# Kernel tuning notes

Hardware: AMD Instinct MI355X
Metric: run time of the kernel (lower is better)

Reference implementation:

```python
import jax, jax.numpy as jnp
import numpy as np

ALPHA = 0.5      # GCN2Conv alpha
THETA = 1.0      # GCN2Conv theta (beta_l = log(theta/l + 1))
EPS = 1e-5       # pyg LayerNorm eps
N_LAYERS = 8
N, E, DIN, DHID, DOUT = 50000, 800000, 128, 256, 128


def setup_inputs() -> dict:
    key = jax.random.key(0)
    ks = jax.random.split(key, 10)
    x = jax.random.normal(ks[0], (N, DIN), jnp.float32)
    edge_index = jax.random.randint(ks[1], (2, E), 0, N, dtype=jnp.int32)
    lin1_w = jax.random.normal(ks[2], (DIN, DHID), jnp.float32) / np.sqrt(DIN)
    lin1_b = jnp.zeros((DHID,), jnp.float32)
    conv_w1 = jax.random.normal(ks[3], (N_LAYERS, DHID, DHID), jnp.float32) / np.sqrt(DHID)
    conv_w2 = jax.random.normal(ks[4], (N_LAYERS, DHID, DHID), jnp.float32) / np.sqrt(DHID)
    norm_gamma = jnp.ones((N_LAYERS, DHID), jnp.float32)
    norm_beta = jnp.zeros((N_LAYERS, DHID), jnp.float32)
    lin2_w = jax.random.normal(ks[5], (DHID, DOUT), jnp.float32) / np.sqrt(DHID)
    lin2_b = jnp.zeros((DOUT,), jnp.float32)
    return {"x": x, "edge_index": edge_index, "lin1_w": lin1_w, "lin1_b": lin1_b,
            "conv_w1": conv_w1, "conv_w2": conv_w2, "norm_gamma": norm_gamma,
            "norm_beta": norm_beta, "lin2_w": lin2_w, "lin2_b": lin2_b}


def _gcn_norm(edge_index, n_nodes, dtype):
    # add self loops, then symmetric deg^{-1/2} A_hat deg^{-1/2} normalization
    loop = jnp.arange(n_nodes, dtype=edge_index.dtype)
    row = jnp.concatenate([edge_index[0], loop])
    col = jnp.concatenate([edge_index[1], loop])
    deg = jax.ops.segment_sum(jnp.ones_like(row, dtype=dtype), col, num_segments=n_nodes)
    dis = jnp.where(deg > 0, jax.lax.rsqrt(jnp.maximum(deg, 1e-12)), 0.0)
    return row, col, dis[row] * dis[col]


def _graph_layernorm(h, gamma, beta):
    # pyg LayerNorm mode='graph', batch=None: normalize over all nodes+features
    z = h - jnp.mean(h)
    z = z / (jnp.sqrt(jnp.mean(z * z)) + EPS)
    return gamma * z + beta


def reference(x, edge_index, lin1_w, lin1_b, conv_w1, conv_w2, norm_gamma, norm_beta, lin2_w, lin2_b):
    n_nodes = x.shape[0]
    row, col, enorm = _gcn_norm(edge_index, n_nodes, x.dtype)
    # lin1 + relu (dropout p=0 -> identity); residual=None -> zeros
    x0 = jax.nn.relu(x @ lin1_w + lin1_b)
    h = x0
    for i in range(conv_w1.shape[0]):
        beta_l = float(np.log(THETA / (i + 1) + 1.0))
        # sparse neighborhood aggregation: out[c] += norm * h[r]
        agg = jax.ops.segment_sum(h[row] * enorm[:, None], col, num_segments=n_nodes)
        t = (1.0 - ALPHA) * agg          # propagated part
        r = ALPHA * x0                   # initial-residual part (res = x0 + zeros)
        # shared_weights=False: separate weights for propagated and residual parts
        h = (1.0 - beta_l) * (t + r) + beta_l * (t @ conv_w1[i] + r @ conv_w2[i])
        h = jax.nn.relu(_graph_layernorm(h, norm_gamma[i], norm_beta[i]))
    return jax.nn.relu(h @ lin2_w + lin2_b)
```

## Files before the change

kernel.cpp:

```cpp
#include <hip/hip_runtime.h>
#include <hip/hip_bf16.h>
#include <math.h>

#define DIN 128
#define DH 256
#define DOUT 128
#define NLAYERS 8
#define EPSLN 1e-5f

typedef __hip_bfloat16 bf16;
typedef __attribute__((ext_vector_type(8))) short short8;
typedef __attribute__((ext_vector_type(4))) short short4v;
typedef __attribute__((ext_vector_type(4))) float f32x4;

__device__ __forceinline__ float ldf(const void* p, size_t idx, int isbf) {
    if (isbf) return __bfloat162float(((const bf16*)p)[idx]);
    return ((const float*)p)[idx];
}
__device__ __forceinline__ short f2s(float v) {
    bf16 b = __float2bfloat16(v);
    return *reinterpret_cast<short*>(&b);
}
__device__ __forceinline__ float s2f(short s) {
    unsigned int u = ((unsigned int)(unsigned short)s) << 16;
    float f;
    __builtin_memcpy(&f, &u, 4);
    return f;
}
__device__ __forceinline__ void gl_lds16(const void* g, void* l) {
    __builtin_amdgcn_global_load_lds(
        (const __attribute__((address_space(1))) unsigned int*)g,
        (__attribute__((address_space(3))) unsigned int*)l,
        16, 0, 0);
}

__global__ void k_detect(const unsigned int* __restrict__ xw, int* __restrict__ flag) {
    __shared__ int cnt;
    if (threadIdx.x == 0) cnt = 0;
    __syncthreads();
    unsigned int w = xw[threadIdx.x];
    int e = (w >> 7) & 0xFF;
    if (e >= 112 && e <= 140) atomicAdd(&cnt, 1);
    __syncthreads();
    if (threadIdx.x == 0) *flag = (cnt >= 128) ? 1 : 0;
}

__global__ void k_init_cnt(int* __restrict__ cnt, float* __restrict__ stats, int N) {
    int i = blockIdx.x * blockDim.x + threadIdx.x;
    if (i < N) cnt[i] = 0;
    if (blockIdx.x == 0 && threadIdx.x < 16) stats[threadIdx.x] = 0.0f;
}
__global__ void k_count(const int* __restrict__ cols, int* __restrict__ cnt, int E) {
    int e = blockIdx.x * blockDim.x + threadIdx.x;
    if (e < E) atomicAdd(&cnt[cols[e]], 1);
}
__global__ void k_dis(const int* __restrict__ cnt, float* __restrict__ dis, int N) {
    int i = blockIdx.x * blockDim.x + threadIdx.x;
    if (i < N) dis[i] = rsqrtf(1.0f + (float)cnt[i]);
}
__global__ void k_scan1(const int* __restrict__ cnt, int* __restrict__ rowptr,
                        int* __restrict__ bsum, int N) {
    __shared__ int s[256];
    int t = threadIdx.x;
    int i = blockIdx.x * 256 + t;
    s[t] = (i < N) ? cnt[i] : 0;
    __syncthreads();
    for (int off = 1; off < 256; off <<= 1) {
        int x = (t >= off) ? s[t - off] : 0;
        __syncthreads();
        s[t] += x;
        __syncthreads();
    }
    if (i < N) rowptr[i + 1] = s[t];
    if (t == 255) bsum[blockIdx.x] = s[255];
}
__global__ void k_scan2(int* __restrict__ bsum, int nb) {
    __shared__ int s[256];
    int t = threadIdx.x;
    s[t] = (t < nb) ? bsum[t] : 0;
    __syncthreads();
    for (int off = 1; off < 256; off <<= 1) {
        int x = (t >= off) ? s[t - off] : 0;
        __syncthreads();
        s[t] += x;
        __syncthreads();
    }
    if (t < nb) bsum[t] = s[t];
}
__global__ void k_scan3(int* __restrict__ rowptr, const int* __restrict__ bsum,
                        int* __restrict__ cursor, int N) {
    int i = blockIdx.x * 256 + threadIdx.x;
    if (i == 0) { rowptr[0] = 0; cursor[0] = 0; }
    if (i < N) {
        int v = rowptr[i + 1] + ((blockIdx.x > 0) ? bsum[blockIdx.x - 1] : 0);
        rowptr[i + 1] = v;
        cursor[i + 1] = v;
    }
}
__global__ void k_fill(const int* __restrict__ rows, const int* __restrict__ cols,
                       int* __restrict__ cursor, int* __restrict__ csr, int E) {
    int e = blockIdx.x * blockDim.x + threadIdx.x;
    if (e < E) {
        int c = cols[e], r = rows[e];
        int pos = atomicAdd(&cursor[c], 1);
        csr[pos] = r;
    }
}

__global__ void k_transw2(const void* __restrict__ w1, const void* __restrict__ w2,
                          const int* __restrict__ flag, short* __restrict__ wt) {
    __shared__ float tile[32][33];
    int z = blockIdx.z;
    int lay = z >> 1, m = z & 1;
    const void* src = m ? w2 : w1;
    size_t sbase = (size_t)lay * 65536;
    short* dst = wt + (size_t)lay * 131072 + (size_t)m * 256;
    float bl = logf(1.0f / (float)(lay + 1) + 1.0f);
    float c0 = 0.5f * (1.0f - bl);
    float c1 = 0.5f * bl;
    int isbf = *flag;
    int tx = threadIdx.x, ty = threadIdx.y;
    int n0 = blockIdx.x * 32, k0 = blockIdx.y * 32;
    #pragma unroll
    for (int i = 0; i < 4; i++) {
        int k = k0 + ty + i * 8;
        tile[ty + i * 8][tx] = ldf(src, sbase + (size_t)k * 256 + n0 + tx, isbf);
    }
    __syncthreads();
    #pragma unroll
    for (int i = 0; i < 4; i++) {
        int n = n0 + ty + i * 8;
        int k = k0 + tx;
        float v = c1 * tile[tx][ty + i * 8];
        if (k == n) v += c0;
        dst[(size_t)n * 512 + k] = f2s(v);
    }
}

__global__ void k_transw_lin(const void* __restrict__ src, const int* __restrict__ flag,
                             short* __restrict__ dst, int K, int Nc) {
    __shared__ float tile[32][33];
    int isbf = *flag;
    int tx = threadIdx.x, ty = threadIdx.y;
    int n0 = blockIdx.x * 32, k0 = blockIdx.y * 32;
    #pragma unroll
    for (int i = 0; i < 4; i++) {
        int k = k0 + ty + i * 8;
        tile[ty + i * 8][tx] = ldf(src, (size_t)k * Nc + n0 + tx, isbf);
    }
    __syncthreads();
    #pragma unroll
    for (int i = 0; i < 4; i++) {
        int n = n0 + ty + i * 8;
        dst[(size_t)n * K + k0 + tx] = f2s(tile[tx][ty + i * 8]);
    }
}

__global__ void k_convx(const void* __restrict__ x, const int* __restrict__ flag,
                        short* __restrict__ xb, int total) {
    int i = blockIdx.x * 256 + threadIdx.x;
    if (i < total) xb[i] = f2s(ldf(x, i, *flag));
}

template<int KK, int FINAL, int TRANSA>
__global__ __launch_bounds__(256) void gemm_mfma(
    const short* __restrict__ A, const short* __restrict__ wt,
    const void* __restrict__ bias, const int* __restrict__ flag,
    const void* __restrict__ g, const void* __restrict__ b, size_t loff,
    const float* __restrict__ stats2, float invTotal,
    void* __restrict__ outp, int Nn)
{
    __shared__ __align__(16) short Atile[128 * 32];
    __shared__ __align__(16) short Btile[128 * 32];
    int t = threadIdx.x;
    int w = t >> 6, lane = t & 63;
    int lr = lane & 15, quad = lane >> 4;
    int row0 = blockIdx.x * 128;
    int col0 = blockIdx.y * 128;
    int ncols = gridDim.y * 128;
    int sub = t & 3;
    int srow = t >> 2;
    const int isbf = *flag;
    float mu = 0.f, inv = 0.f;
    if (TRANSA) {
        mu = stats2[0] * invTotal;
        float var = stats2[1] * invTotal - mu * mu;
        var = var > 0.f ? var : 0.f;
        inv = 1.0f / (sqrtf(var) + EPSLN);
    }
    f32x4 acc[2][8];
    #pragma unroll
    for (int m = 0; m < 2; m++)
        #pragma unroll
        for (int nt = 0; nt < 8; nt++)
            #pragma unroll
            for (int j = 0; j < 4; j++) acc[m][nt][j] = 0.f;

    for (int kb = 0; kb < KK; kb += 32) {
        #pragma unroll
        for (int r = 0; r < 2; r++) {
            int gr = row0 + srow + r * 64;
            if (gr >= Nn) gr = Nn - 1;
            if (TRANSA) {
                short8 av = *(const short8*)(A + (size_t)gr * KK + kb + sub * 8);
                short8 tv;
                #pragma unroll
                for (int j = 0; j < 8; j++) {
                    int kc = kb + sub * 8 + j;
                    float gg = ldf(g, loff + kc, isbf);
                    float bb = ldf(b, loff + kc, isbf);
                    float v = fmaf(gg * inv, s2f(av[j]), fmaf(-gg * inv, mu, bb));
                    v = v > 0.f ? v : 0.f;
                    tv[j] = f2s(v);
                }
                *(short8*)(Atile + (size_t)(t + r * 256) * 8) = tv;
            } else {
                gl_lds16(A + (size_t)gr * KK + kb + sub * 8,
                         Atile + (size_t)(t + r * 256) * 8);
            }
        }
        #pragma unroll
        for (int r = 0; r < 2; r++) {
            int n = col0 + srow + r * 64;
            gl_lds16(wt + (size_t)n * KK + kb + sub * 8,
                     Btile + (size_t)(t + r * 256) * 8);
        }
        __syncthreads();
        short8 a0 = *(const short8*)(Atile + (w * 32 + lr) * 32 + quad * 8);
        short8 a1 = *(const short8*)(Atile + (w * 32 + 16 + lr) * 32 + quad * 8);
        #pragma unroll
        for (int nt = 0; nt < 8; nt++) {
            short8 bv = *(const short8*)(Btile + (nt * 16 + lr) * 32 + quad * 8);
            acc[0][nt] = __builtin_amdgcn_mfma_f32_16x16x32_bf16(a0, bv, acc[0][nt], 0, 0, 0);
            acc[1][nt] = __builtin_amdgcn_mfma_f32_16x16x32_bf16(a1, bv, acc[1][nt], 0, 0, 0);
        }
        __syncthreads();
    }
    #pragma unroll
    for (int m = 0; m < 2; m++) {
        #pragma unroll
        for (int nt = 0; nt < 8; nt++) {
            int gc = col0 + nt * 16 + lr;
            float bb = ldf(bias, gc, isbf);
            #pragma unroll
            for (int i = 0; i < 4; i++) {
                int gr = row0 + w * 32 + m * 16 + quad * 4 + i;
                if (gr < Nn) {
                    float v = acc[m][nt][i] + bb;
                    v = v > 0.f ? v : 0.f;
                    size_t off = (size_t)gr * ncols + gc;
                    if (FINAL) {
                        if (isbf) ((bf16*)outp)[off] = __float2bfloat16(v);
                        else      ((float*)outp)[off] = v;
                    } else {
                        ((bf16*)outp)[off] = __float2bfloat16(v);
                    }
                }
            }
        }
    }
}

__global__ __launch_bounds__(256) void k_gather5(
    const int* __restrict__ rowptr, const int* __restrict__ csr,
    const float* __restrict__ dis, const bf16* __restrict__ hsrc,
    bf16* __restrict__ agg,
    const void* __restrict__ g, const void* __restrict__ b, size_t loff,
    const float* __restrict__ stats2, float invTotal, int useLN,
    const int* __restrict__ flag, int N)
{
    int gid = blockIdx.x * 256 + threadIdx.x;
    int node = gid >> 6;
    if (node >= N) return;
    int col = (gid & 63) * 4;
    float cA[4], cB[4];
    if (useLN) {
        int isbf = *flag;
        float mu = stats2[0] * invTotal;
        float var = stats2[1] * invTotal - mu * mu;
        var = var > 0.f ? var : 0.f;
        float inv = 1.0f / (sqrtf(var) + EPSLN);
        #pragma unroll
        for (int j = 0; j < 4; j++) {
            float gg = ldf(g, loff + col + j, isbf);
            float bb = ldf(b, loff + col + j, isbf);
            cA[j] = gg * inv;
            cB[j] = fmaf(-gg * inv, mu, bb);
        }
    } else {
        #pragma unroll
        for (int j = 0; j < 4; j++) { cA[j] = 1.0f; cB[j] = 0.0f; }
    }
    const short* hs = (const short*)hsrc;
    float dc = dis[node];
    float a0[4], a1[4], a2[4], a3[4];
    {
        short4v hv = *(const short4v*)(hs + (size_t)node * DH + col);
        #pragma unroll
        for (int j = 0; j < 4; j++) {
            float v = fmaf(cA[j], s2f(hv[j]), cB[j]);
            v = v > 0.f ? v : 0.f;
            a0[j] = dc * v;
            a1[j] = 0.f; a2[j] = 0.f; a3[j] = 0.f;
        }
    }
    int i = rowptr[node], e1 = rowptr[node + 1];
    for (; i + 8 <= e1; i += 8) {
        int r0 = csr[i],     r1 = csr[i + 1], r2 = csr[i + 2], r3 = csr[i + 3];
        int r4 = csr[i + 4], r5 = csr[i + 5], r6 = csr[i + 6], r7 = csr[i + 7];
        float w0 = dis[r0], w1 = dis[r1], w2 = dis[r2], w3 = dis[r3];
        float w4 = dis[r4], w5 = dis[r5], w6 = dis[r6], w7 = dis[r7];
        short4v v0 = *(const short4v*)(hs + (size_t)r0 * DH + col);
        short4v v1 = *(const short4v*)(hs + (size_t)r1 * DH + col);
        short4v v2 = *(const short4v*)(hs + (size_t)r2 * DH + col);
        short4v v3 = *(const short4v*)(hs + (size_t)r3 * DH + col);
        short4v v4 = *(const short4v*)(hs + (size_t)r4 * DH + col);
        short4v v5 = *(const short4v*)(hs + (size_t)r5 * DH + col);
        short4v v6 = *(const short4v*)(hs + (size_t)r6 * DH + col);
        short4v v7 = *(const short4v*)(hs + (size_t)r7 * DH + col);
        #pragma unroll
        for (int j = 0; j < 4; j++) {
            float t0 = fmaf(cA[j], s2f(v0[j]), cB[j]); t0 = t0 > 0.f ? t0 : 0.f;
            float t1 = fmaf(cA[j], s2f(v1[j]), cB[j]); t1 = t1 > 0.f ? t1 : 0.f;
            float t2 = fmaf(cA[j], s2f(v2[j]), cB[j]); t2 = t2 > 0.f ? t2 : 0.f;
            float t3 = fmaf(cA[j], s2f(v3[j]), cB[j]); t3 = t3 > 0.f ? t3 : 0.f;
            float t4 = fmaf(cA[j], s2f(v4[j]), cB[j]); t4 = t4 > 0.f ? t4 : 0.f;
            float t5 = fmaf(cA[j], s2f(v5[j]), cB[j]); t5 = t5 > 0.f ? t5 : 0.f;
            float t6 = fmaf(cA[j], s2f(v6[j]), cB[j]); t6 = t6 > 0.f ? t6 : 0.f;
            float t7 = fmaf(cA[j], s2f(v7[j]), cB[j]); t7 = t7 > 0.f ? t7 : 0.f;
            a0[j] = fmaf(w0, t0, a0[j]);
            a1[j] = fmaf(w1, t1, a1[j]);
            a2[j] = fmaf(w2, t2, a2[j]);
            a3[j] = fmaf(w3, t3, a3[j]);
            a0[j] = fmaf(w4, t4, a0[j]);
            a1[j] = fmaf(w5, t5, a1[j]);
            a2[j] = fmaf(w6, t6, a2[j]);
            a3[j] = fmaf(w7, t7, a3[j]);
        }
    }
    for (; i + 2 <= e1; i += 2) {
        int r0 = csr[i], r1 = csr[i + 1];
        float w0 = dis[r0], w1 = dis[r1];
        short4v v0 = *(const short4v*)(hs + (size_t)r0 * DH + col);
        short4v v1 = *(const short4v*)(hs + (size_t)r1 * DH + col);
        #pragma unroll
        for (int j = 0; j < 4; j++) {
            float t0 = fmaf(cA[j], s2f(v0[j]), cB[j]); t0 = t0 > 0.f ? t0 : 0.f;
            float t1 = fmaf(cA[j], s2f(v1[j]), cB[j]); t1 = t1 > 0.f ? t1 : 0.f;
            a0[j] = fmaf(w0, t0, a0[j]);
            a1[j] = fmaf(w1, t1, a1[j]);
        }
    }
    for (; i < e1; i++) {
        int r = csr[i];
        float wr = dis[r];
        short4v v0 = *(const short4v*)(hs + (size_t)r * DH + col);
        #pragma unroll
        for (int j = 0; j < 4; j++) {
            float t0 = fmaf(cA[j], s2f(v0[j]), cB[j]); t0 = t0 > 0.f ? t0 : 0.f;
            a0[j] = fmaf(wr, t0, a0[j]);
        }
    }
    short4v o;
    #pragma unroll
    for (int j = 0; j < 4; j++) o[j] = f2s(dc * ((a0[j] + a1[j]) + (a2[j] + a3[j])));
    *(short4v*)((short*)agg + (size_t)node * DH + col) = o;
}

__global__ __launch_bounds__(256) void gemm_layer4(
    const bf16* __restrict__ agg, const bf16* __restrict__ x0,
    const short* __restrict__ wt, bf16* __restrict__ h,
    float* __restrict__ stats2, int Nn)
{
    __shared__ __align__(16) short Atile[128 * 32];
    __shared__ __align__(16) short Btile[128 * 32];
    __shared__ float red[512];
    int t = threadIdx.x;
    int w = t >> 6, lane = t & 63;
    int lr = lane & 15, quad = lane >> 4;
    int row0 = blockIdx.x * 128;
    int col0 = blockIdx.y * 128;
    int sub = t & 3;
    int srow = t >> 2;
    f32x4 acc[2][8];
    #pragma unroll
    for (int m = 0; m < 2; m++)
        #pragma unroll
        for (int nt = 0; nt < 8; nt++)
            #pragma unroll
            for (int j = 0; j < 4; j++) acc[m][nt][j] = 0.f;

    for (int kb = 0; kb < 512; kb += 32) {
        const short* Asrc = (const short*)((kb < DH) ? agg : x0);
        int ka = kb & (DH - 1);
        #pragma unroll
        for (int r = 0; r < 2; r++) {
            int gr = row0 + srow + r * 64;
            if (gr >= Nn) gr = Nn - 1;
            gl_lds16(Asrc + (size_t)gr * DH + ka + sub * 8,
                     Atile + (size_t)(t + r * 256) * 8);
        }
        #pragma unroll
        for (int r = 0; r < 2; r++) {
            int n = col0 + srow + r * 64;
            gl_lds16(wt + (size_t)n * 512 + kb + sub * 8,
                     Btile + (size_t)(t + r * 256) * 8);
        }
        __syncthreads();
        short8 a0 = *(const short8*)(Atile + (w * 32 + lr) * 32 + quad * 8);
        short8 a1 = *(const short8*)(Atile + (w * 32 + 16 + lr) * 32 + quad * 8);
        #pragma unroll
        for (int nt = 0; nt < 8; nt++) {
            short8 bv = *(const short8*)(Btile + (nt * 16 + lr) * 32 + quad * 8);
            acc[0][nt] = __builtin_amdgcn_mfma_f32_16x16x32_bf16(a0, bv, acc[0][nt], 0, 0, 0);
            acc[1][nt] = __builtin_amdgcn_mfma_f32_16x16x32_bf16(a1, bv, acc[1][nt], 0, 0, 0);
        }
        __syncthreads();
    }
    float lsum = 0.f, lsq = 0.f;
    #pragma unroll
    for (int m = 0; m < 2; m++) {
        #pragma unroll
        for (int nt = 0; nt < 8; nt++) {
            int gc = col0 + nt * 16 + lr;
            #pragma unroll
            for (int i = 0; i < 4; i++) {
                int gr = row0 + w * 32 + m * 16 + quad * 4 + i;
                if (gr < Nn) {
                    float v = acc[m][nt][i];
                    h[(size_t)gr * DH + gc] = __float2bfloat16(v);
                    lsum += v;
                    lsq += v * v;
                }
            }
        }
    }
    red[t] = lsum;
    red[256 + t] = lsq;
    __syncthreads();
    for (int s = 128; s > 0; s >>= 1) {
        if (t < s) { red[t] += red[t + s]; red[256 + t] += red[256 + t + s]; }
        __syncthreads();
    }
    if (t == 0) {
        atomicAdd(&stats2[0], red[0]);
        atomicAdd(&stats2[1], red[256]);
    }
}

extern "C" void kernel_launch(void* const* d_in, const int* in_sizes, int n_in,
                              void* d_out, int out_size, void* d_ws, size_t ws_size,
                              hipStream_t stream) {
    const void* x      = d_in[0];
    const int*  ei     = (const int*)d_in[1];
    const void* lin1_w = d_in[2];
    const void* lin1_b = d_in[3];
    const void* conv_w1= d_in[4];
    const void* conv_w2= d_in[5];
    const void* gam    = d_in[6];
    const void* bet    = d_in[7];
    const void* lin2_w = d_in[8];
    const void* lin2_b = d_in[9];

    const int N = in_sizes[0] / DIN;
    const int E = in_sizes[1] / 2;
    const int* rows = ei;
    const int* cols = ei + E;
    const size_t NDH = (size_t)N * DH;
    const size_t Nr = ((size_t)N + 255) / 256 * 256;

    char* p = (char*)d_ws;
    auto alloc = [&](size_t bytes) { char* q = p; p += (bytes + 255) & ~(size_t)255; return q; };
    float* dis    = (float*)alloc(Nr * 4);
    float* stats  = (float*)alloc(1024);
    int*   flag   = (int*)(stats + 16);
    int*   cnt    = (int*)alloc(Nr * 4);
    int*   rowptr = (int*)alloc((Nr + 256) * 4);
    int*   cursor = (int*)alloc((Nr + 256) * 4);
    int*   bsum   = (int*)alloc(1024);
    int*   csr    = (int*)alloc((size_t)E * 4);
    short* wt     = (short*)alloc((size_t)NLAYERS * 131072 * 2);
    short* w1t    = (short*)alloc((size_t)DH * DIN * 2);
    short* w2t    = (short*)alloc((size_t)DOUT * DH * 2);
    short* xb     = (short*)alloc((size_t)N * DIN * 2);
    bf16*  agg    = (bf16*)alloc(NDH * 2);
    bf16*  x0     = (bf16*)alloc(NDH * 2);
    bf16*  h      = (bf16*)alloc(NDH * 2);

    dim3 blk(256);
    int nbN = (N + 255) / 256;
    dim3 gN(nbN);
    dim3 gE((E + 255) / 256);
    dim3 gB128_2((N + 127) / 128, 2);
    dim3 gB128_1((N + 127) / 128, 1);
    dim3 gG((N + 3) / 4);
    dim3 gTW(8, 8, 16);
    dim3 bTW(32, 8);

    k_detect<<<1, 256, 0, stream>>>((const unsigned int*)x, flag);
    k_init_cnt<<<gN, blk, 0, stream>>>(cnt, stats, N);
    k_count<<<gE, blk, 0, stream>>>(cols, cnt, E);
    k_dis<<<gN, blk, 0, stream>>>(cnt, dis, N);
    k_scan1<<<gN, blk, 0, stream>>>(cnt, rowptr, bsum, N);
    k_scan2<<<1, 256, 0, stream>>>(bsum, nbN);
    k_scan3<<<gN, blk, 0, stream>>>(rowptr, bsum, cursor, N);
    k_fill<<<gE, blk, 0, stream>>>(rows, cols, cursor, csr, E);
    k_transw2<<<gTW, bTW, 0, stream>>>(conv_w1, conv_w2, flag, wt);
    k_transw_lin<<<dim3(DH / 32, DIN / 32), bTW, 0, stream>>>(lin1_w, flag, w1t, DIN, DH);
    k_transw_lin<<<dim3(DOUT / 32, DH / 32), bTW, 0, stream>>>(lin2_w, flag, w2t, DH, DOUT);
    k_convx<<<dim3((unsigned)(((size_t)N * DIN + 255) / 256)), blk, 0, stream>>>(x, flag, xb, N * DIN);

    gemm_mfma<DIN, 0, 0><<<gB128_2, blk, 0, stream>>>(xb, w1t, lin1_b, flag,
                                                      nullptr, nullptr, 0, stats, 0.f,
                                                      x0, N);

    const float invTotal = 1.0f / ((float)N * (float)DH);
    for (int l = 0; l < NLAYERS; l++) {
        const bf16* hsrc = (l == 0) ? x0 : h;
        size_t loff = (l == 0) ? 0 : (size_t)(l - 1) * DH;
        const float* st = (l == 0) ? stats : stats + 2 * (l - 1);
        k_gather5<<<gG, blk, 0, stream>>>(rowptr, csr, dis, hsrc, agg,
                                          gam, bet, loff, st, invTotal,
                                          l > 0 ? 1 : 0, flag, N);
        gemm_layer4<<<gB128_2, blk, 0, stream>>>(agg, x0, wt + (size_t)l * 131072,
                                                 h, stats + 2 * l, N);
    }
    gemm_mfma<DH, 1, 1><<<gB128_1, blk, 0, stream>>>((const short*)h, w2t, lin2_b, flag,
                                                     gam, bet, (size_t)(NLAYERS - 1) * DH,
                                                     stats + 2 * (NLAYERS - 1), invTotal,
                                                     d_out, N);
}
```

Measured before the change: 1.280 ms.

## Fuse all GCN2 layers into one persistent cooperative kernel with grid syncs

Replaces the per-layer gather and GEMM launches with a single cooperative persistent kernel. Each layer runs an in-place layernorm+ReLU pass over h, a wave-per-node gather, and a 64-row-tile MFMA GEMM, separated by grid-wide syncs. The goal is to remove the 16 kernel launches and their tail effects, but it adds an extra full read/write pass for normalisation and three grid barriers per layer. The smaller GEMM tile and a grid capped at 768 blocks may lower per-tile efficiency, and the fallback gather loses its 8-way unroll.

```diff
diff --git a/kernel.cpp b/kernel.cpp
--- a/kernel.cpp
+++ b/kernel.cpp
@@ -1,6 +1,9 @@
 #include <hip/hip_runtime.h>
+#include <hip/hip_cooperative_groups.h>
 #include <hip/hip_bf16.h>
 #include <math.h>
+
+namespace cg = cooperative_groups;
 
 #define DIN 128
 #define DH 256
@@ -293,7 +296,7 @@
     }
     const short* hs = (const short*)hsrc;
     float dc = dis[node];
-    float a0[4], a1[4], a2[4], a3[4];
+    float a0[4], a1[4];
     {
         short4v hv = *(const short4v*)(hs + (size_t)node * DH + col);
         #pragma unroll
@@ -301,43 +304,10 @@
             float v = fmaf(cA[j], s2f(hv[j]), cB[j]);
             v = v > 0.f ? v : 0.f;
             a0[j] = dc * v;
-            a1[j] = 0.f; a2[j] = 0.f; a3[j] = 0.f;
+            a1[j] = 0.f;
         }
     }
     int i = rowptr[node], e1 = rowptr[node + 1];
-    for (; i + 8 <= e1; i += 8) {
-        int r0 = csr[i],     r1 = csr[i + 1], r2 = csr[i + 2], r3 = csr[i + 3];
-        int r4 = csr[i + 4], r5 = csr[i + 5], r6 = csr[i + 6], r7 = csr[i + 7];
-        float w0 = dis[r0], w1 = dis[r1], w2 = dis[r2], w3 = dis[r3];
-        float w4 = dis[r4], w5 = dis[r5], w6 = dis[r6], w7 = dis[r7];
-        short4v v0 = *(const short4v*)(hs + (size_t)r0 * DH + col);
-        short4v v1 = *(const short4v*)(hs + (size_t)r1 * DH + col);
-        short4v v2 = *(const short4v*)(hs + (size_t)r2 * DH + col);
-        short4v v3 = *(const short4v*)(hs + (size_t)r3 * DH + col);
-        short4v v4 = *(const short4v*)(hs + (size_t)r4 * DH + col);
-        short4v v5 = *(const short4v*)(hs + (size_t)r5 * DH + col);
-        short4v v6 = *(const short4v*)(hs + (size_t)r6 * DH + col);
-        short4v v7 = *(const short4v*)(hs + (size_t)r7 * DH + col);
-        #pragma unroll
-        for (int j = 0; j < 4; j++) {
-            float t0 = fmaf(cA[j], s2f(v0[j]), cB[j]); t0 = t0 > 0.f ? t0 : 0.f;
-            float t1 = fmaf(cA[j], s2f(v1[j]), cB[j]); t1 = t1 > 0.f ? t1 : 0.f;
-            float t2 = fmaf(cA[j], s2f(v2[j]), cB[j]); t2 = t2 > 0.f ? t2 : 0.f;
-            float t3 = fmaf(cA[j], s2f(v3[j]), cB[j]); t3 = t3 > 0.f ? t3 : 0.f;
-            float t4 = fmaf(cA[j], s2f(v4[j]), cB[j]); t4 = t4 > 0.f ? t4 : 0.f;
-            float t5 = fmaf(cA[j], s2f(v5[j]), cB[j]); t5 = t5 > 0.f ? t5 : 0.f;
-            float t6 = fmaf(cA[j], s2f(v6[j]), cB[j]); t6 = t6 > 0.f ? t6 : 0.f;
-            float t7 = fmaf(cA[j], s2f(v7[j]), cB[j]); t7 = t7 > 0.f ? t7 : 0.f;
-            a0[j] = fmaf(w0, t0, a0[j]);
-            a1[j] = fmaf(w1, t1, a1[j]);
-            a2[j] = fmaf(w2, t2, a2[j]);
-            a3[j] = fmaf(w3, t3, a3[j]);
-            a0[j] = fmaf(w4, t4, a0[j]);
-            a1[j] = fmaf(w5, t5, a1[j]);
-            a2[j] = fmaf(w6, t6, a2[j]);
-            a3[j] = fmaf(w7, t7, a3[j]);
-        }
-    }
     for (; i + 2 <= e1; i += 2) {
         int r0 = csr[i], r1 = csr[i + 1];
         float w0 = dis[r0], w1 = dis[r1];
@@ -363,7 +333,7 @@
     }
     short4v o;
     #pragma unroll
-    for (int j = 0; j < 4; j++) o[j] = f2s(dc * ((a0[j] + a1[j]) + (a2[j] + a3[j])));
+    for (int j = 0; j < 4; j++) o[j] = f2s(dc * (a0[j] + a1[j]));
     *(short4v*)((short*)agg + (size_t)node * DH + col) = o;
 }
 
@@ -448,6 +418,186 @@
     }
 }
 
+__global__ __launch_bounds__(256, 2) void k_layers(
+    const int* __restrict__ rowptr, const int* __restrict__ csr,
+    const float* __restrict__ dis, const short* __restrict__ x0s,
+    short* __restrict__ hs, short* __restrict__ aggs,
+    const short* __restrict__ wt,
+    const void* __restrict__ gam, const void* __restrict__ bet,
+    float* __restrict__ stats, const int* __restrict__ flag,
+    float invTotal, int N)
+{
+    cg::grid_group grid = cg::this_grid();
+    __shared__ __align__(16) short Atile[64 * 32];
+    __shared__ __align__(16) short Btile[128 * 32];
+    __shared__ float red[512];
+    const int t = threadIdx.x;
+    const int w = t >> 6, lane = t & 63;
+    const int lr = lane & 15, quad = lane >> 4;
+    const int isbf = *flag;
+    const int nthreads = gridDim.x * 256;
+    const int gtid = blockIdx.x * 256 + t;
+    const int nwaves = gridDim.x * 4;
+    const int waveId = blockIdx.x * 4 + w;
+    const int srow = t >> 2, sub = t & 3;
+    const size_t NDH8 = (size_t)N * 32;
+    const int ntiles = ((N + 63) >> 6) * 2;
+
+    for (int l = 0; l < NLAYERS; ++l) {
+        if (l > 0) {
+            const float* st = stats + 2 * (l - 1);
+            size_t loff = (size_t)(l - 1) * DH;
+            float mu = st[0] * invTotal;
+            float var = st[1] * invTotal - mu * mu;
+            var = var > 0.f ? var : 0.f;
+            float inv = 1.0f / (sqrtf(var) + EPSLN);
+            for (size_t c = (size_t)gtid; c < NDH8; c += nthreads) {
+                int colb = (int)((c & 31) * 8);
+                short8 v = *(short8*)(hs + c * 8);
+                short8 o;
+                #pragma unroll
+                for (int j = 0; j < 8; j++) {
+                    float gg = ldf(gam, loff + colb + j, isbf);
+                    float bb = ldf(bet, loff + colb + j, isbf);
+                    float xv = fmaf(gg * inv, s2f(v[j]), fmaf(-gg * inv, mu, bb));
+                    xv = xv > 0.f ? xv : 0.f;
+                    o[j] = f2s(xv);
+                }
+                *(short8*)(hs + c * 8) = o;
+            }
+            __threadfence();
+            grid.sync();
+        }
+        {
+            const short* src = (l == 0) ? x0s : hs;
+            int col = lane * 4;
+            for (int node = waveId; node < N; node += nwaves) {
+                float dc = dis[node];
+                float a0[4], a1[4], a2[4], a3[4];
+                short4v hv = *(const short4v*)(src + (size_t)node * DH + col);
+                #pragma unroll
+                for (int j = 0; j < 4; j++) {
+                    a0[j] = dc * s2f(hv[j]);
+                    a1[j] = 0.f; a2[j] = 0.f; a3[j] = 0.f;
+                }
+                int i = rowptr[node], e1 = rowptr[node + 1];
+                for (; i + 8 <= e1; i += 8) {
+                    int r0 = csr[i],     r1 = csr[i + 1], r2 = csr[i + 2], r3 = csr[i + 3];
+                    int r4 = csr[i + 4], r5 = csr[i + 5], r6 = csr[i + 6], r7 = csr[i + 7];
+                    float w0 = dis[r0], w1 = dis[r1], w2 = dis[r2], w3 = dis[r3];
+                    float w4 = dis[r4], w5 = dis[r5], w6 = dis[r6], w7 = dis[r7];
+                    short4v v0 = *(const short4v*)(src + (size_t)r0 * DH + col);
+                    short4v v1 = *(const short4v*)(src + (size_t)r1 * DH + col);
+                    short4v v2 = *(const short4v*)(src + (size_t)r2 * DH + col);
+                    short4v v3 = *(const short4v*)(src + (size_t)r3 * DH + col);
+                    short4v v4 = *(const short4v*)(src + (size_t)r4 * DH + col);
+                    short4v v5 = *(const short4v*)(src + (size_t)r5 * DH + col);
+                    short4v v6 = *(const short4v*)(src + (size_t)r6 * DH + col);
+                    short4v v7 = *(const short4v*)(src + (size_t)r7 * DH + col);
+                    #pragma unroll
+                    for (int j = 0; j < 4; j++) {
+                        a0[j] = fmaf(w0, s2f(v0[j]), a0[j]);
+                        a1[j] = fmaf(w1, s2f(v1[j]), a1[j]);
+                        a2[j] = fmaf(w2, s2f(v2[j]), a2[j]);
+                        a3[j] = fmaf(w3, s2f(v3[j]), a3[j]);
+                        a0[j] = fmaf(w4, s2f(v4[j]), a0[j]);
+                        a1[j] = fmaf(w5, s2f(v5[j]), a1[j]);
+                        a2[j] = fmaf(w6, s2f(v6[j]), a2[j]);
+                        a3[j] = fmaf(w7, s2f(v7[j]), a3[j]);
+                    }
+                }
+                for (; i + 2 <= e1; i += 2) {
+                    int r0 = csr[i], r1 = csr[i + 1];
+                    float w0 = dis[r0], w1 = dis[r1];
+                    short4v v0 = *(const short4v*)(src + (size_t)r0 * DH + col);
+                    short4v v1 = *(const short4v*)(src + (size_t)r1 * DH + col);
+                    #pragma unroll
+                    for (int j = 0; j < 4; j++) {
+                        a0[j] = fmaf(w0, s2f(v0[j]), a0[j]);
+                        a1[j] = fmaf(w1, s2f(v1[j]), a1[j]);
+                    }
+                }
+                for (; i < e1; i++) {
+                    int r = csr[i];
+                    float wr = dis[r];
+                    short4v v0 = *(const short4v*)(src + (size_t)r * DH + col);
+                    #pragma unroll
+                    for (int j = 0; j < 4; j++) a0[j] = fmaf(wr, s2f(v0[j]), a0[j]);
+                }
+                short4v o;
+                #pragma unroll
+                for (int j = 0; j < 4; j++)
+                    o[j] = f2s(dc * ((a0[j] + a1[j]) + (a2[j] + a3[j])));
+                *(short4v*)(aggs + (size_t)node * DH + col) = o;
+            }
+        }
+        __threadfence();
+        grid.sync();
+        {
+            const short* wl = wt + (size_t)l * 131072;
+            float lsum = 0.f, lsq = 0.f;
+            for (int tile = blockIdx.x; tile < ntiles; tile += gridDim.x) {
+                int row0 = (tile >> 1) * 64;
+                int col0 = (tile & 1) * 128;
+                f32x4 acc[8];
+                #pragma unroll
+                for (int nt = 0; nt < 8; nt++)
+                    #pragma unroll
+                    for (int j = 0; j < 4; j++) acc[nt][j] = 0.f;
+                for (int kb = 0; kb < 512; kb += 32) {
+                    const short* Asrc = (kb < DH) ? aggs : x0s;
+                    int ka = kb & (DH - 1);
+                    int gr = row0 + srow;
+                    if (gr >= N) gr = N - 1;
+                    gl_lds16(Asrc + (size_t)gr * DH + ka + sub * 8,
+                             Atile + (size_t)t * 8);
+                    #pragma unroll
+                    for (int r = 0; r < 2; r++) {
+                        int n = col0 + srow + r * 64;
+                        gl_lds16(wl + (size_t)n * 512 + kb + sub * 8,
+                                 Btile + (size_t)(t + r * 256) * 8);
+                    }
+                    __syncthreads();
+                    short8 a0 = *(const short8*)(Atile + (w * 16 + lr) * 32 + quad * 8);
+                    #pragma unroll
+                    for (int nt = 0; nt < 8; nt++) {
+                        short8 bv = *(const short8*)(Btile + (nt * 16 + lr) * 32 + quad * 8);
+                        acc[nt] = __builtin_amdgcn_mfma_f32_16x16x32_bf16(a0, bv, acc[nt], 0, 0, 0);
+                    }
+                    __syncthreads();
+                }
+                #pragma unroll
+                for (int nt = 0; nt < 8; nt++) {
+                    int gc = col0 + nt * 16 + lr;
+                    #pragma unroll
+                    for (int i = 0; i < 4; i++) {
+                        int gr = row0 + w * 16 + quad * 4 + i;
+                        if (gr < N) {
+                            float v = acc[nt][i];
+                            hs[(size_t)gr * DH + gc] = f2s(v);
+                            lsum += v;
+                            lsq += v * v;
+                        }
+                    }
+                }
+            }
+            red[t] = lsum;
+            red[256 + t] = lsq;
+            __syncthreads();
+            for (int s = 128; s > 0; s >>= 1) {
+                if (t < s) { red[t] += red[t + s]; red[256 + t] += red[256 + t + s]; }
+                __syncthreads();
+            }
+            if (t == 0) {
+                atomicAdd(&stats[2 * l], red[0]);
+                atomicAdd(&stats[2 * l + 1], red[256]);
+            }
+        }
+        __threadfence();
+        grid.sync();
+    }
+}
+
 extern "C" void kernel_launch(void* const* d_in, const int* in_sizes, int n_in,
                               void* d_out, int out_size, void* d_ws, size_t ws_size,
                               hipStream_t stream) {
@@ -483,9 +633,9 @@
     short* w1t    = (short*)alloc((size_t)DH * DIN * 2);
     short* w2t    = (short*)alloc((size_t)DOUT * DH * 2);
     short* xb     = (short*)alloc((size_t)N * DIN * 2);
-    bf16*  agg    = (bf16*)alloc(NDH * 2);
-    bf16*  x0     = (bf16*)alloc(NDH * 2);
-    bf16*  h      = (bf16*)alloc(NDH * 2);
+    short* aggs   = (short*)alloc(NDH * 2);
+    short* x0s    = (short*)alloc(NDH * 2);
+    short* hs     = (short*)alloc(NDH * 2);
 
     dim3 blk(256);
     int nbN = (N + 255) / 256;
@@ -512,20 +662,52 @@
 
     gemm_mfma<DIN, 0, 0><<<gB128_2, blk, 0, stream>>>(xb, w1t, lin1_b, flag,
                                                       nullptr, nullptr, 0, stats, 0.f,
-                                                      x0, N);
-
-    const float invTotal = 1.0f / ((float)N * (float)DH);
-    for (int l = 0; l < NLAYERS; l++) {
-        const bf16* hsrc = (l == 0) ? x0 : h;
-        size_t loff = (l == 0) ? 0 : (size_t)(l - 1) * DH;
-        const float* st = (l == 0) ? stats : stats + 2 * (l - 1);
-        k_gather5<<<gG, blk, 0, stream>>>(rowptr, csr, dis, hsrc, agg,
-                                          gam, bet, loff, st, invTotal,
-                                          l > 0 ? 1 : 0, flag, N);
-        gemm_layer4<<<gB128_2, blk, 0, stream>>>(agg, x0, wt + (size_t)l * 131072,
-                                                 h, stats + 2 * l, N);
-    }
-    gemm_mfma<DH, 1, 1><<<gB128_1, blk, 0, stream>>>((const short*)h, w2t, lin2_b, flag,
+                                                      (void*)x0s, N);
+
+    float invTotal = 1.0f / ((float)N * (float)DH);
+    int Nn = N;
+
+    int occ = 0;
+    hipError_t orc = hipOccupancyMaxActiveBlocksPerMultiprocessor(
+        &occ, (const void*)k_layers, 256, 0);
+    int grid = (orc == hipSuccess && occ > 0) ? occ * 256 : 0;
+    if (grid > 768) grid = 768;
+
+    hipError_t rc = hipErrorUnknown;
+    if (grid > 0) {
+        const int* a_rowptr = rowptr;
+        const int* a_csr = csr;
+        const float* a_dis = dis;
+        const short* a_x0 = x0s;
+        short* a_h = hs;
+        short* a_agg = aggs;
+        const short* a_wt = wt;
+        const void* a_gam = gam;
+        const void* a_bet = bet;
+        float* a_stats = stats;
+        const int* a_flag = flag;
+        void* args[] = { (void*)&a_rowptr, (void*)&a_csr, (void*)&a_dis,
+                         (void*)&a_x0, (void*)&a_h, (void*)&a_agg, (void*)&a_wt,
+                         (void*)&a_gam, (void*)&a_bet, (void*)&a_stats,
+                         (void*)&a_flag, (void*)&invTotal, (void*)&Nn };
+        rc = hipLaunchCooperativeKernel((const void*)k_layers, dim3(grid), dim3(256),
+                                        args, 0, stream);
+    }
+    if (rc != hipSuccess) {
+        for (int l = 0; l < NLAYERS; l++) {
+            const bf16* hsrc = (const bf16*)((l == 0) ? x0s : hs);
+            size_t loff = (l == 0) ? 0 : (size_t)(l - 1) * DH;
+            const float* st = (l == 0) ? stats : stats + 2 * (l - 1);
+            k_gather5<<<gG, blk, 0, stream>>>(rowptr, csr, dis, hsrc, (bf16*)aggs,
+                                              gam, bet, loff, st, invTotal,
+                                              l > 0 ? 1 : 0, flag, N);
+            gemm_layer4<<<gB128_2, blk, 0, stream>>>((const bf16*)aggs, (const bf16*)x0s,
+                                                     wt + (size_t)l * 131072,
+                                                     (bf16*)hs, stats + 2 * l, N);
+        }
+    }
+
+    gemm_mfma<DH, 1, 1><<<gB128_1, blk, 0, stream>>>(hs, w2t, lin2_b, flag,
                                                      gam, bet, (size_t)(NLAYERS - 1) * DH,
                                                      stats + 2 * (NLAYERS - 1), invTotal,
                                                      d_out, N);
```

Result: slower. 4.209 ms (+228.8%).
